# Kernel optimization log

Hardware: AMD Instinct MI355X
Metric: run time of the kernel (lower is better)

The kernel has to match this reference:

```python
import jax, jax.numpy as jnp
import numpy as np


def setup_inputs() -> dict:
    key = jax.random.key(0)
    k1, k2, k3, k4 = jax.random.split(key, 4)
    B, T, L, C, F = 1024, 128, 256, 2, 784
    x = jax.random.normal(k1, (B, T, F), dtype=jnp.float32)
    W = jax.random.normal(k2, (L, F), dtype=jnp.float32) * (1.0 / np.sqrt(F))
    b = jax.random.normal(k3, (L,), dtype=jnp.float32) * 0.01
    contribution = jax.random.normal(k4, (T, L, C), dtype=jnp.float32)
    return {"x": x, "W": W, "b": b, "contribution": contribution}


def reference(x, W, b, contribution):
    # symbolic_paths: Linear(784 -> leaf) + Hardtanh  -> [B, T, L]
    sp = jnp.clip(jnp.einsum('btf,lf->btl', x, W) + b, -1.0, 1.0)
    # per-(tree,leaf) outer product: class_value[b,t,l,c] = sp[b,t,l] * contribution[t,l,c]
    cv = sp[..., None] * contribution[None]          # [B, T, L, C]
    p = jax.nn.softmax(cv, axis=-1)                  # softmax over classes
    gini = jnp.sum(1.0 - p * p, axis=-1)             # [B, T, L]
    return (sp, gini)
```

## Files before the change

kernel.cpp:

```cpp
#include <hip/hip_runtime.h>
#include <hip/hip_bf16.h>

typedef __attribute__((ext_vector_type(8))) short bf16x8;
typedef __attribute__((ext_vector_type(4))) float f32x4;

#define B_SZ   1024
#define T_SZ   128
#define L_SZ   256
#define F_SZ   784
#define M_TOT  (B_SZ * T_SZ)
#define BK     32
#define KSTEPS 25

#define WPRE_ELEMS (KSTEPS * 4 * L_SZ)
#define WPRE_BYTES (WPRE_ELEMS * 16)
#define CDIFF_ELEMS (T_SZ * L_SZ)
#define WS_NEED (WPRE_BYTES + CDIFF_ELEMS * 4)

#define ROWB    656
#define ABF_OFF 21504
#define SMEM_SZ 33792

__device__ __forceinline__ unsigned short f2bf(float f) {
    __hip_bfloat16 h = __float2bfloat16(f);
    return *reinterpret_cast<unsigned short*>(&h);
}

__global__ __launch_bounds__(256) void dn_prep(
    const float* __restrict__ W, const float* __restrict__ contrib,
    unsigned short* __restrict__ wpre, float* __restrict__ cdiff)
{
    const int gid = blockIdx.x * 256 + threadIdx.x;
    if (gid < WPRE_ELEMS) {
        const int leaf = gid & 255;
        const int kg   = (gid >> 8) & 3;
        const int ks   = gid >> 10;
        const int k0   = ks * BK + kg * 8;
        bf16x8 v;
        #pragma unroll
        for (int j = 0; j < 8; ++j) {
            const int k = k0 + j;
            const float f = (k < F_SZ) ? W[(size_t)leaf * F_SZ + k] : 0.f;
            v[j] = (short)f2bf(f);
        }
        *reinterpret_cast<bf16x8*>(wpre + (size_t)gid * 8) = v;
    } else {
        const int cid = gid - WPRE_ELEMS;
        if (cid < CDIFF_ELEMS)
            cdiff[cid] = contrib[(size_t)cid * 2] - contrib[(size_t)cid * 2 + 1];
    }
}


#define GLDS(g, l)                                                           \
    __builtin_amdgcn_global_load_lds(                                        \
        (const __attribute__((address_space(1))) void*)(g),                  \
        (__attribute__((address_space(3))) void*)(l), 16, 0, 0)

__global__ __launch_bounds__(512, 6) void dn_fused13(
    const float* __restrict__ x, const unsigned short* __restrict__ wpre,
    const float* __restrict__ bias, const float* __restrict__ cdiff,
    float* __restrict__ out)
{
    __shared__ __align__(16) unsigned char smem[SMEM_SZ];

    const int tid  = threadIdx.x;
    const int lane = tid & 63;
    const int wid  = tid >> 6;
    const int lr   = lane & 15;
    const int kseg = lane >> 4;

    const int rowBase = blockIdx.x * 32;
    const int colBase = wid * 32;

    const char* xb = (const char*)x;
    const char* srcB[3];
    const char* srcC[3];
    bool        v4[3];
    #pragma unroll
    for (int jj = 0; jj < 3; ++jj) {
        const int j = wid + 8 * jj;
        const unsigned s    = j * 1024 + lane * 16;
        const unsigned row  = s / ROWB;
        const unsigned colb = s - row * ROWB;
        const bool     ok   = (row < 32) && (colb < 640);
        const unsigned rcl  = (row < 32) ? row : 0;
        srcC[jj] = xb + (size_t)(rowBase + rcl) * 3136;
        srcB[jj] = srcC[jj] + (ok ? colb : 0);
        v4[jj]   = ok && (colb < 576);
    }

    #define ISSUE(w) do {                                                    \
        _Pragma("unroll")                                                    \
        for (int _jj = 0; _jj < 3; ++_jj) {                                  \
            const int _j = wid + 8 * _jj;                                    \
            if (_j < 21) {                                                   \
                const char* _s = ((w) < 4) ? (srcB[_jj] + (w) * 640)         \
                                : (v4[_jj] ? srcB[_jj] + 2560 : srcC[_jj]);  \
                GLDS(_s, smem + _j * 1024);                                  \
            }                                                                \
        }                                                                    \
    } while (0)

    #define CVT() do {                                                       \
        _Pragma("unroll")                                                    \
        for (int _h = 0; _h < 2; ++_h) {                                     \
            const int _c = tid + _h * 512;                                   \
            if (_c < 640) {                                                  \
                const int _row = _c / 20;                                    \
                const int _kc  = _c - _row * 20;                             \
                const f32x4 _lo = *reinterpret_cast<const f32x4*>(           \
                    smem + _row * ROWB + _kc * 32);                          \
                const f32x4 _hi = *reinterpret_cast<const f32x4*>(           \
                    smem + _row * ROWB + _kc * 32 + 16);                     \
                bf16x8 _v;                                                   \
                _Pragma("unroll")                                            \
                for (int _j = 0; _j < 4; ++_j) {                             \
                    _v[_j]     = (short)f2bf(_lo[_j]);                       \
                    _v[4 + _j] = (short)f2bf(_hi[_j]);                       \
                }                                                            \
                *reinterpret_cast<bf16x8*>(smem + ABF_OFF                    \
                    + (_kc * 33 + _row) * 16) = _v;                          \
            }                                                                \
        }                                                                    \
    } while (0)

    f32x4 acc[2][2];
    #pragma unroll
    for (int mi = 0; mi < 2; ++mi)
        #pragma unroll
        for (int ni = 0; ni < 2; ++ni)
            acc[mi][ni] = (f32x4){0.f, 0.f, 0.f, 0.f};

    const unsigned short* wpb = wpre + ((size_t)kseg * L_SZ + colBase + lr) * 8;
    bf16x8 wcur[2], wnxt[2];

    ISSUE(0);
    wcur[0] = *reinterpret_cast<const bf16x8*>(wpb);
    wcur[1] = *reinterpret_cast<const bf16x8*>(wpb + 128);
    __syncthreads();
    CVT();
    __syncthreads();
    ISSUE(1);

    #pragma unroll
    for (int w = 0; w < 5; ++w) {
        #pragma unroll
        for (int i = 0; i < 5; ++i) {
            const int ks = w * 5 + i;
            if (ks + 1 < KSTEPS) {
                wnxt[0] = *reinterpret_cast<const bf16x8*>(wpb + (size_t)(ks + 1) * 8192);
                wnxt[1] = *reinterpret_cast<const bf16x8*>(wpb + (size_t)(ks + 1) * 8192 + 128);
            }
            bf16x8 af[2];
            #pragma unroll
            for (int m = 0; m < 2; ++m)
                af[m] = *reinterpret_cast<const bf16x8*>(
                    smem + ABF_OFF + (((i * 4 + kseg) * 33) + m * 16 + lr) * 16);

            acc[0][0] = __builtin_amdgcn_mfma_f32_16x16x32_bf16(af[0], wcur[0], acc[0][0], 0, 0, 0);
            acc[0][1] = __builtin_amdgcn_mfma_f32_16x16x32_bf16(af[0], wcur[1], acc[0][1], 0, 0, 0);
            acc[1][0] = __builtin_amdgcn_mfma_f32_16x16x32_bf16(af[1], wcur[0], acc[1][0], 0, 0, 0);
            acc[1][1] = __builtin_amdgcn_mfma_f32_16x16x32_bf16(af[1], wcur[1], acc[1][1], 0, 0, 0);
            wcur[0] = wnxt[0];
            wcur[1] = wnxt[1];
        }
        if (w < 4) {
            __syncthreads();
            CVT();
            __syncthreads();
            if (w < 3) ISSUE(w + 2);
        }
    }
    #undef ISSUE
    #undef CVT

    float spv[2][2][4];
    #pragma unroll
    for (int ni = 0; ni < 2; ++ni) {
        const float bb = bias[colBase + ni * 16 + lr];
        #pragma unroll
        for (int mi = 0; mi < 2; ++mi)
            #pragma unroll
            for (int r = 0; r < 4; ++r)
                spv[mi][ni][r] = fminf(fmaxf(acc[mi][ni][r] + bb, -1.f), 1.f);
    }

    typedef float OtRow[264];
    OtRow* Ot = reinterpret_cast<OtRow*>(smem);

    const int erow = tid >> 4;
    const int ecol = (tid & 15) * 4;
    const size_t GOFF = (size_t)M_TOT * L_SZ;
    float* orow = out + (size_t)(rowBase + erow) * L_SZ;

    __syncthreads();

    #pragma unroll
    for (int ni = 0; ni < 2; ++ni)
        #pragma unroll
        for (int mi = 0; mi < 2; ++mi)
            #pragma unroll
            for (int r = 0; r < 4; ++r)
                Ot[mi * 16 + kseg * 4 + r][colBase + ni * 16 + lr] = spv[mi][ni][r];
    __syncthreads();
    #pragma unroll
    for (int j = 0; j < 4; ++j) {
        const f32x4 v = *reinterpret_cast<const f32x4*>(&Ot[erow][ecol + 64 * j]);
        *reinterpret_cast<f32x4*>(orow + ecol + 64 * j) = v;
    }
    __syncthreads();

    #pragma unroll
    for (int ni = 0; ni < 2; ++ni) {
        const int col = colBase + ni * 16 + lr;
        #pragma unroll
        for (int mi = 0; mi < 2; ++mi)
            #pragma unroll
            for (int r = 0; r < 4; ++r) {
                const int t = (rowBase + mi * 16 + kseg * 4 + r) & (T_SZ - 1);
                const float d  = spv[mi][ni][r] * cdiff[t * L_SZ + col];
                const float ed = __expf(d);
                const float s2 = ed / (1.f + ed);
                Ot[mi * 16 + kseg * 4 + r][col] = fmaf(2.f * s2, 1.f - s2, 1.f);
            }
    }
    __syncthreads();
    #pragma unroll
    for (int j = 0; j < 4; ++j) {
        const f32x4 v = *reinterpret_cast<const f32x4*>(&Ot[erow][ecol + 64 * j]);
        *reinterpret_cast<f32x4*>(orow + GOFF + ecol + 64 * j) = v;
    }
}

__global__ __launch_bounds__(512) void dn_fused_v1(
    const float* __restrict__ x, const float* __restrict__ W,
    const float* __restrict__ bias, const float* __restrict__ contrib,
    float* __restrict__ out)
{
    __shared__ bf16x8 As[4][128];
    __shared__ bf16x8 Bs[4][L_SZ];

    const int tid    = threadIdx.x;
    const int lane   = tid & 63;
    const int wid    = tid >> 6;
    const int waveM  = wid >> 2;
    const int waveN  = wid & 3;
    const int blkRow = blockIdx.x * 128;
    const int ar = tid >> 2;
    const int ak = (tid & 3) * 8;
    const int wr = tid >> 1;
    const int wk = (tid & 1) * 16;
    const int laneRow = lane & 15;
    const int kgrp    = lane >> 4;

    f32x4 acc[4][4];
    #pragma unroll
    for (int i = 0; i < 4; ++i)
        #pragma unroll
        for (int j = 0; j < 4; ++j)
            acc[i][j] = (f32x4){0.f, 0.f, 0.f, 0.f};

    const float* xrow = x + (size_t)(blkRow + ar) * F_SZ;
    const float* wrow = W + (size_t)wr * F_SZ;
    const f32x4 zf = {0.f, 0.f, 0.f, 0.f};

    f32x4 xa0 = *reinterpret_cast<const f32x4*>(xrow + ak);
    f32x4 xa1 = *reinterpret_cast<const f32x4*>(xrow + ak + 4);
    f32x4 wa0 = *reinterpret_cast<const f32x4*>(wrow + wk);
    f32x4 wa1 = *reinterpret_cast<const f32x4*>(wrow + wk + 4);
    f32x4 wa2 = *reinterpret_cast<const f32x4*>(wrow + wk + 8);
    f32x4 wa3 = *reinterpret_cast<const f32x4*>(wrow + wk + 12);

    for (int ks = 0; ks < KSTEPS; ++ks) {
        bf16x8 av, wv0, wv1;
        #pragma unroll
        for (int j = 0; j < 4; ++j) {
            av[j]      = (short)f2bf(xa0[j]);
            av[4 + j]  = (short)f2bf(xa1[j]);
            wv0[j]     = (short)f2bf(wa0[j]);
            wv0[4 + j] = (short)f2bf(wa1[j]);
            wv1[j]     = (short)f2bf(wa2[j]);
            wv1[4 + j] = (short)f2bf(wa3[j]);
        }
        As[ak >> 3][ar] = av;
        Bs[wk >> 3][wr] = wv0;
        Bs[(wk >> 3) + 1][wr] = wv1;
        __syncthreads();

        if (ks + 1 < KSTEPS) {
            const int kb = (ks + 1) * BK;
            if (kb + ak < F_SZ) {
                xa0 = *reinterpret_cast<const f32x4*>(xrow + kb + ak);
                xa1 = *reinterpret_cast<const f32x4*>(xrow + kb + ak + 4);
            } else { xa0 = zf; xa1 = zf; }
            if (kb + wk < F_SZ) {
                wa0 = *reinterpret_cast<const f32x4*>(wrow + kb + wk);
                wa1 = *reinterpret_cast<const f32x4*>(wrow + kb + wk + 4);
                wa2 = *reinterpret_cast<const f32x4*>(wrow + kb + wk + 8);
                wa3 = *reinterpret_cast<const f32x4*>(wrow + kb + wk + 12);
            } else { wa0 = zf; wa1 = zf; wa2 = zf; wa3 = zf; }
        }

        bf16x8 af[4], bfv[4];
        #pragma unroll
        for (int mi = 0; mi < 4; ++mi)
            af[mi] = As[kgrp][waveM * 64 + mi * 16 + laneRow];
        #pragma unroll
        for (int ni = 0; ni < 4; ++ni)
            bfv[ni] = Bs[kgrp][waveN * 64 + ni * 16 + laneRow];
        #pragma unroll
        for (int mi = 0; mi < 4; ++mi)
            #pragma unroll
            for (int ni = 0; ni < 4; ++ni)
                acc[mi][ni] = __builtin_amdgcn_mfma_f32_16x16x32_bf16(
                    af[mi], bfv[ni], acc[mi][ni], 0, 0, 0);
        __syncthreads();
    }

    const size_t GOFF  = (size_t)M_TOT * L_SZ;
    const int    rbase = waveM * 64 + (lane >> 4) * 4;
    const int    cbase = waveN * 64 + laneRow;
    #pragma unroll
    for (int ni = 0; ni < 4; ++ni) {
        const int col = cbase + ni * 16;
        const float bb = bias[col];
        #pragma unroll
        for (int mi = 0; mi < 4; ++mi) {
            #pragma unroll
            for (int r = 0; r < 4; ++r) {
                const int m = blkRow + rbase + mi * 16 + r;
                const int t = m & (T_SZ - 1);
                float v  = acc[mi][ni][r] + bb;
                float sp = fminf(fmaxf(v, -1.f), 1.f);
                const float* cp = contrib + (size_t)(t * L_SZ + col) * 2;
                const float d  = sp * (cp[0] - cp[1]);
                const float ed = __expf(d);
                const float s  = ed / (1.f + ed);
                const float g  = fmaf(2.f * s, 1.f - s, 1.f);
                const size_t o = (size_t)m * L_SZ + col;
                out[o]        = sp;
                out[GOFF + o] = g;
            }
        }
    }
}

extern "C" void kernel_launch(void* const* d_in, const int* in_sizes, int n_in,
                              void* d_out, int out_size, void* d_ws, size_t ws_size,
                              hipStream_t stream) {
    const float* x       = (const float*)d_in[0];
    const float* W       = (const float*)d_in[1];
    const float* bias    = (const float*)d_in[2];
    const float* contrib = (const float*)d_in[3];
    float* out = (float*)d_out;

    if (ws_size >= (size_t)WS_NEED && d_ws != nullptr) {
        unsigned short* wpre  = (unsigned short*)d_ws;
        float*          cdiff = (float*)((char*)d_ws + WPRE_BYTES);
        const int prep_threads = WPRE_ELEMS + CDIFF_ELEMS;
        dn_prep<<<(prep_threads + 255) / 256, 256, 0, stream>>>(W, contrib, wpre, cdiff);
        dn_fused13<<<M_TOT / 32, 512, 0, stream>>>(x, wpre, bias, cdiff, out);
    } else {
        dn_fused_v1<<<M_TOT / 128, 512, 0, stream>>>(x, W, bias, contrib, out);
    }
}
```

Before: 187.6 us.

## Process four row strips per block with cross-strip prefetch of x

Each block now handles 128 rows as four 32-row strips in a loop instead of one strip, launching 1024 blocks instead of 4096. The first x chunk of the next strip is issued during the last k-window of the current strip, overlapping loads with the epilogue. The output staging buffer moves to the bf16 region and is written in two 16-row halves, with LDS grown slightly. This cuts block launch and prologue overhead but adds more barriers per strip and reduces grid parallelism.

```diff
diff --git a/kernel.cpp b/kernel.cpp
--- a/kernel.cpp
+++ b/kernel.cpp
@@ -19,7 +19,8 @@
 
 #define ROWB    656
 #define ABF_OFF 21504
-#define SMEM_SZ 33792
+#define SMEM_SZ 38400
+#define STRIPB  100352
 
 __device__ __forceinline__ unsigned short f2bf(float f) {
     __hip_bfloat16 h = __float2bfloat16(f);
@@ -57,7 +58,7 @@
         (const __attribute__((address_space(1))) void*)(g),                  \
         (__attribute__((address_space(3))) void*)(l), 16, 0, 0)
 
-__global__ __launch_bounds__(512, 6) void dn_fused13(
+__global__ __launch_bounds__(512, 6) void dn_fused14(
     const float* __restrict__ x, const unsigned short* __restrict__ wpre,
     const float* __restrict__ bias, const float* __restrict__ cdiff,
     float* __restrict__ out)
@@ -70,34 +71,25 @@
     const int lr   = lane & 15;
     const int kseg = lane >> 4;
 
-    const int rowBase = blockIdx.x * 32;
-    const int colBase = wid * 32;
-
-    const char* xb = (const char*)x;
-    const char* srcB[3];
-    const char* srcC[3];
-    bool        v4[3];
-    #pragma unroll
-    for (int jj = 0; jj < 3; ++jj) {
-        const int j = wid + 8 * jj;
-        const unsigned s    = j * 1024 + lane * 16;
-        const unsigned row  = s / ROWB;
-        const unsigned colb = s - row * ROWB;
-        const bool     ok   = (row < 32) && (colb < 640);
-        const unsigned rcl  = (row < 32) ? row : 0;
-        srcC[jj] = xb + (size_t)(rowBase + rcl) * 3136;
-        srcB[jj] = srcC[jj] + (ok ? colb : 0);
-        v4[jj]   = ok && (colb < 576);
-    }
-
-    #define ISSUE(w) do {                                                    \
+    const int bid      = blockIdx.x;
+    const int colBase  = wid * 32;
+    const char* xbase0 = (const char*)x + (size_t)bid * 128 * 3136;
+
+    #define ISSUE(w, soff) do {                                              \
         _Pragma("unroll")                                                    \
         for (int _jj = 0; _jj < 3; ++_jj) {                                  \
             const int _j = wid + 8 * _jj;                                    \
             if (_j < 21) {                                                   \
-                const char* _s = ((w) < 4) ? (srcB[_jj] + (w) * 640)         \
-                                : (v4[_jj] ? srcB[_jj] + 2560 : srcC[_jj]);  \
-                GLDS(_s, smem + _j * 1024);                                  \
+                const unsigned _s    = _j * 1024 + lane * 16;                \
+                const unsigned _row  = _s / ROWB;                            \
+                const unsigned _colb = _s - _row * ROWB;                     \
+                const bool     _ok   = (_row < 32) && (_colb < 640);         \
+                const unsigned _rcl  = (_row < 32) ? _row : 0;               \
+                const char* _base = xbase0 + (soff) + (size_t)_rcl * 3136;   \
+                const char* _src;                                            \
+                if ((w) < 4) _src = _base + (_ok ? _colb : 0) + (w) * 640;   \
+                else _src = _base + ((_ok && _colb < 576) ? 2560 + _colb : 0);\
+                GLDS(_src, smem + _j * 1024);                                \
             }                                                                \
         }                                                                    \
     } while (0)
@@ -125,112 +117,114 @@
         }                                                                    \
     } while (0)
 
-    f32x4 acc[2][2];
-    #pragma unroll
-    for (int mi = 0; mi < 2; ++mi)
-        #pragma unroll
-        for (int ni = 0; ni < 2; ++ni)
-            acc[mi][ni] = (f32x4){0.f, 0.f, 0.f, 0.f};
-
     const unsigned short* wpb = wpre + ((size_t)kseg * L_SZ + colBase + lr) * 8;
-    bf16x8 wcur[2], wnxt[2];
-
-    ISSUE(0);
-    wcur[0] = *reinterpret_cast<const bf16x8*>(wpb);
-    wcur[1] = *reinterpret_cast<const bf16x8*>(wpb + 128);
-    __syncthreads();
-    CVT();
-    __syncthreads();
-    ISSUE(1);
-
-    #pragma unroll
-    for (int w = 0; w < 5; ++w) {
-        #pragma unroll
-        for (int i = 0; i < 5; ++i) {
-            const int ks = w * 5 + i;
-            if (ks + 1 < KSTEPS) {
-                wnxt[0] = *reinterpret_cast<const bf16x8*>(wpb + (size_t)(ks + 1) * 8192);
-                wnxt[1] = *reinterpret_cast<const bf16x8*>(wpb + (size_t)(ks + 1) * 8192 + 128);
+    typedef float OtRow16[264];
+    OtRow16* Ot = reinterpret_cast<OtRow16*>(smem + ABF_OFF);
+    const int erow = tid >> 5;
+    const int ecol = (tid & 31) * 8;
+    const size_t GOFF = (size_t)M_TOT * L_SZ;
+
+    ISSUE(0, 0);
+
+    for (int st = 0; st < 4; ++st) {
+        const int    rowBase = bid * 128 + st * 32;
+        const size_t soff    = (size_t)st * STRIPB;
+
+        __syncthreads();
+        CVT();
+        __syncthreads();
+        ISSUE(1, soff);
+
+        f32x4 acc[2][2];
+        #pragma unroll
+        for (int mi = 0; mi < 2; ++mi)
+            #pragma unroll
+            for (int ni = 0; ni < 2; ++ni)
+                acc[mi][ni] = (f32x4){0.f, 0.f, 0.f, 0.f};
+
+        bf16x8 wcur[2], wnxt[2];
+        wcur[0] = *reinterpret_cast<const bf16x8*>(wpb);
+        wcur[1] = *reinterpret_cast<const bf16x8*>(wpb + 128);
+
+        #pragma unroll
+        for (int w = 0; w < 5; ++w) {
+            #pragma unroll
+            for (int i = 0; i < 5; ++i) {
+                const int ks = w * 5 + i;
+                if (ks + 1 < KSTEPS) {
+                    wnxt[0] = *reinterpret_cast<const bf16x8*>(wpb + (size_t)(ks + 1) * 8192);
+                    wnxt[1] = *reinterpret_cast<const bf16x8*>(wpb + (size_t)(ks + 1) * 8192 + 128);
+                }
+                bf16x8 af[2];
+                #pragma unroll
+                for (int m = 0; m < 2; ++m)
+                    af[m] = *reinterpret_cast<const bf16x8*>(
+                        smem + ABF_OFF + (((i * 4 + kseg) * 33) + m * 16 + lr) * 16);
+
+                acc[0][0] = __builtin_amdgcn_mfma_f32_16x16x32_bf16(af[0], wcur[0], acc[0][0], 0, 0, 0);
+                acc[0][1] = __builtin_amdgcn_mfma_f32_16x16x32_bf16(af[0], wcur[1], acc[0][1], 0, 0, 0);
+                acc[1][0] = __builtin_amdgcn_mfma_f32_16x16x32_bf16(af[1], wcur[0], acc[1][0], 0, 0, 0);
+                acc[1][1] = __builtin_amdgcn_mfma_f32_16x16x32_bf16(af[1], wcur[1], acc[1][1], 0, 0, 0);
+                wcur[0] = wnxt[0];
+                wcur[1] = wnxt[1];
             }
-            bf16x8 af[2];
-            #pragma unroll
-            for (int m = 0; m < 2; ++m)
-                af[m] = *reinterpret_cast<const bf16x8*>(
-                    smem + ABF_OFF + (((i * 4 + kseg) * 33) + m * 16 + lr) * 16);
-
-            acc[0][0] = __builtin_amdgcn_mfma_f32_16x16x32_bf16(af[0], wcur[0], acc[0][0], 0, 0, 0);
-            acc[0][1] = __builtin_amdgcn_mfma_f32_16x16x32_bf16(af[0], wcur[1], acc[0][1], 0, 0, 0);
-            acc[1][0] = __builtin_amdgcn_mfma_f32_16x16x32_bf16(af[1], wcur[0], acc[1][0], 0, 0, 0);
-            acc[1][1] = __builtin_amdgcn_mfma_f32_16x16x32_bf16(af[1], wcur[1], acc[1][1], 0, 0, 0);
-            wcur[0] = wnxt[0];
-            wcur[1] = wnxt[1];
-        }
-        if (w < 4) {
+            if (w < 4) {
+                __syncthreads();
+                CVT();
+                __syncthreads();
+                if (w < 3)       ISSUE(w + 2, soff);
+                else if (st < 3) ISSUE(0, soff + STRIPB);
+            }
+        }
+        __syncthreads();
+
+        float spv[2][2][4];
+        #pragma unroll
+        for (int ni = 0; ni < 2; ++ni) {
+            const float bb = bias[colBase + ni * 16 + lr];
+            #pragma unroll
+            for (int mi = 0; mi < 2; ++mi)
+                #pragma unroll
+                for (int r = 0; r < 4; ++r)
+                    spv[mi][ni][r] = fminf(fmaxf(acc[mi][ni][r] + bb, -1.f), 1.f);
+        }
+
+        #pragma unroll
+        for (int h = 0; h < 2; ++h) {
+            #pragma unroll
+            for (int ni = 0; ni < 2; ++ni)
+                #pragma unroll
+                for (int r = 0; r < 4; ++r)
+                    Ot[kseg * 4 + r][colBase + ni * 16 + lr] = spv[h][ni][r];
             __syncthreads();
-            CVT();
+            float* orow = out + (size_t)(rowBase + h * 16 + erow) * L_SZ + ecol;
+            *reinterpret_cast<f32x4*>(orow)     = *reinterpret_cast<const f32x4*>(&Ot[erow][ecol]);
+            *reinterpret_cast<f32x4*>(orow + 4) = *reinterpret_cast<const f32x4*>(&Ot[erow][ecol + 4]);
             __syncthreads();
-            if (w < 3) ISSUE(w + 2);
+        }
+        #pragma unroll
+        for (int h = 0; h < 2; ++h) {
+            #pragma unroll
+            for (int ni = 0; ni < 2; ++ni) {
+                const int col = colBase + ni * 16 + lr;
+                #pragma unroll
+                for (int r = 0; r < 4; ++r) {
+                    const int t = (rowBase + h * 16 + kseg * 4 + r) & (T_SZ - 1);
+                    const float d  = spv[h][ni][r] * cdiff[t * L_SZ + col];
+                    const float ed = __expf(d);
+                    const float s2 = ed / (1.f + ed);
+                    Ot[kseg * 4 + r][col] = fmaf(2.f * s2, 1.f - s2, 1.f);
+                }
+            }
+            __syncthreads();
+            float* orow = out + GOFF + (size_t)(rowBase + h * 16 + erow) * L_SZ + ecol;
+            *reinterpret_cast<f32x4*>(orow)     = *reinterpret_cast<const f32x4*>(&Ot[erow][ecol]);
+            *reinterpret_cast<f32x4*>(orow + 4) = *reinterpret_cast<const f32x4*>(&Ot[erow][ecol + 4]);
+            if (h == 0 || st < 3) __syncthreads();
         }
     }
     #undef ISSUE
     #undef CVT
-
-    float spv[2][2][4];
-    #pragma unroll
-    for (int ni = 0; ni < 2; ++ni) {
-        const float bb = bias[colBase + ni * 16 + lr];
-        #pragma unroll
-        for (int mi = 0; mi < 2; ++mi)
-            #pragma unroll
-            for (int r = 0; r < 4; ++r)
-                spv[mi][ni][r] = fminf(fmaxf(acc[mi][ni][r] + bb, -1.f), 1.f);
-    }
-
-    typedef float OtRow[264];
-    OtRow* Ot = reinterpret_cast<OtRow*>(smem);
-
-    const int erow = tid >> 4;
-    const int ecol = (tid & 15) * 4;
-    const size_t GOFF = (size_t)M_TOT * L_SZ;
-    float* orow = out + (size_t)(rowBase + erow) * L_SZ;
-
-    __syncthreads();
-
-    #pragma unroll
-    for (int ni = 0; ni < 2; ++ni)
-        #pragma unroll
-        for (int mi = 0; mi < 2; ++mi)
-            #pragma unroll
-            for (int r = 0; r < 4; ++r)
-                Ot[mi * 16 + kseg * 4 + r][colBase + ni * 16 + lr] = spv[mi][ni][r];
-    __syncthreads();
-    #pragma unroll
-    for (int j = 0; j < 4; ++j) {
-        const f32x4 v = *reinterpret_cast<const f32x4*>(&Ot[erow][ecol + 64 * j]);
-        *reinterpret_cast<f32x4*>(orow + ecol + 64 * j) = v;
-    }
-    __syncthreads();
-
-    #pragma unroll
-    for (int ni = 0; ni < 2; ++ni) {
-        const int col = colBase + ni * 16 + lr;
-        #pragma unroll
-        for (int mi = 0; mi < 2; ++mi)
-            #pragma unroll
-            for (int r = 0; r < 4; ++r) {
-                const int t = (rowBase + mi * 16 + kseg * 4 + r) & (T_SZ - 1);
-                const float d  = spv[mi][ni][r] * cdiff[t * L_SZ + col];
-                const float ed = __expf(d);
-                const float s2 = ed / (1.f + ed);
-                Ot[mi * 16 + kseg * 4 + r][col] = fmaf(2.f * s2, 1.f - s2, 1.f);
-            }
-    }
-    __syncthreads();
-    #pragma unroll
-    for (int j = 0; j < 4; ++j) {
-        const f32x4 v = *reinterpret_cast<const f32x4*>(&Ot[erow][ecol + 64 * j]);
-        *reinterpret_cast<f32x4*>(orow + GOFF + ecol + 64 * j) = v;
-    }
 }
 
 __global__ __launch_bounds__(512) void dn_fused_v1(
@@ -360,7 +354,7 @@
         float*          cdiff = (float*)((char*)d_ws + WPRE_BYTES);
         const int prep_threads = WPRE_ELEMS + CDIFF_ELEMS;
         dn_prep<<<(prep_threads + 255) / 256, 256, 0, stream>>>(W, contrib, wpre, cdiff);
-        dn_fused13<<<M_TOT / 32, 512, 0, stream>>>(x, wpre, bias, cdiff, out);
+        dn_fused14<<<1024, 512, 0, stream>>>(x, wpre, bias, cdiff, out);
     } else {
         dn_fused_v1<<<M_TOT / 128, 512, 0, stream>>>(x, W, bias, contrib, out);
     }
```

After: 645.1 us. 3.44x slower.
